# Kernel tuning notes

Measured on AMD Instinct MI355X. Metric: run time of the kernel, lower is better.

Reference implementation:

```python
import jax, jax.numpy as jnp
import numpy as np

N = 100000
E = 1600000
IN_C = 128
HID = 128
OUT_C = 2
EPS = 1e-5


def gcn_conv(x, src, dst, norm, W, b, num_nodes):
    # PyG GCNConv: linear transform then symmetric-normalized scatter-add
    h = x @ W                                  # [N, out]
    msg = h[src] * norm[:, None]               # [E+N, out] gather
    out = jax.ops.segment_sum(msg, dst, num_segments=num_nodes)
    return out + b


def batchnorm_eval(x, gamma, beta, rm, rv):
    inv = gamma / jnp.sqrt(rv + EPS)
    return (x - rm) * inv + beta


def setup_inputs() -> dict:
    key = jax.random.key(0)
    ks = jax.random.split(key, 16)
    x = jax.random.normal(ks[0], (N, IN_C), dtype=jnp.float32)
    edge_index = jax.random.randint(ks[1], (2, E), 0, N, dtype=jnp.int32)
    s = 1.0 / np.sqrt(IN_C)
    W1 = jax.random.uniform(ks[2], (IN_C, HID), jnp.float32, -s, s)
    b1 = jnp.zeros((HID,), jnp.float32)
    g1 = jnp.ones((HID,), jnp.float32)
    be1 = jnp.zeros((HID,), jnp.float32)
    rm1 = jax.random.normal(ks[3], (HID,), jnp.float32) * 0.1
    rv1 = jax.random.uniform(ks[4], (HID,), jnp.float32, 0.5, 1.5)
    s2 = 1.0 / np.sqrt(HID)
    W2 = jax.random.uniform(ks[5], (HID, HID), jnp.float32, -s2, s2)
    b2 = jnp.zeros((HID,), jnp.float32)
    g2 = jnp.ones((HID,), jnp.float32)
    be2 = jnp.zeros((HID,), jnp.float32)
    rm2 = jax.random.normal(ks[6], (HID,), jnp.float32) * 0.1
    rv2 = jax.random.uniform(ks[7], (HID,), jnp.float32, 0.5, 1.5)
    W3 = jax.random.uniform(ks[8], (HID, OUT_C), jnp.float32, -s2, s2)
    b3 = jnp.zeros((OUT_C,), jnp.float32)
    return {"x": x, "edge_index": edge_index,
            "W1": W1, "b1": b1, "g1": g1, "be1": be1, "rm1": rm1, "rv1": rv1,
            "W2": W2, "b2": b2, "g2": g2, "be2": be2, "rm2": rm2, "rv2": rv2,
            "W3": W3, "b3": b3}


def reference(x, edge_index, W1, b1, g1, be1, rm1, rv1,
              W2, b2, g2, be2, rm2, rv2, W3, b3):
    num_nodes = x.shape[0]
    loops = jnp.arange(num_nodes, dtype=edge_index.dtype)
    src = jnp.concatenate([edge_index[0], loops])   # add self loops
    dst = jnp.concatenate([edge_index[1], loops])
    deg = jax.ops.segment_sum(jnp.ones_like(dst, dtype=x.dtype), dst,
                              num_segments=num_nodes)
    dinv = jax.lax.rsqrt(deg)                        # deg >= 1 with self loops
    norm = dinv[src] * dinv[dst]                     # [E+N]

    h = gcn_conv(x, src, dst, norm, W1, b1, num_nodes)
    h = jax.nn.relu(batchnorm_eval(h, g1, be1, rm1, rv1))
    h = gcn_conv(h, src, dst, norm, W2, b2, num_nodes)
    h = jax.nn.relu(batchnorm_eval(h, g2, be2, rm2, rv2))
    out = gcn_conv(h, src, dst, norm, W3, b3, num_nodes)
    return out
```

## Files before the change

### kernel.cpp

```cpp
#include <hip/hip_runtime.h>

#define NN 100000
#define EE 1600000
#define CH 128

typedef _Float16 h2 __attribute__((ext_vector_type(2)));
typedef _Float16 h8 __attribute__((ext_vector_type(8)));
typedef float f32x4 __attribute__((ext_vector_type(4)));

#define S_NODES 512
#define NBUCK 196
#define CAP_E 10240


__global__ __launch_bounds__(256) void k_passA(const int* __restrict__ src, const int* __restrict__ dst,
                                               int* __restrict__ gcur, int* __restrict__ eb) {
    __shared__ int hist[NBUCK];
    __shared__ int curL[NBUCK];
    for (int t = threadIdx.x; t < NBUCK; t += 256) hist[t] = 0;
    __syncthreads();
    int base = blockIdx.x * 4096;
    int pk[16], bk[16];
#pragma unroll
    for (int j = 0; j < 16; ++j) {
        int i = base + threadIdx.x + 256 * j;
        if (i < EE) {
            int s = src[i], d = dst[i];
            bk[j] = d >> 9;
            pk[j] = (s << 9) | (d & 511);
            atomicAdd(&hist[bk[j]], 1);
        } else bk[j] = -1;
    }
    __syncthreads();
    for (int t = threadIdx.x; t < NBUCK; t += 256) {
        int h = hist[t];
        curL[t] = (h > 0) ? atomicAdd(&gcur[t], h) : 0;
    }
    __syncthreads();
#pragma unroll
    for (int j = 0; j < 16; ++j) {
        if (bk[j] >= 0) {
            int pos = atomicAdd(&curL[bk[j]], 1);
            if (pos < CAP_E) eb[bk[j] * CAP_E + pos] = pk[j];
        }
    }
}

__global__ __launch_bounds__(256) void k_passB1(const int* __restrict__ gcur, const int* __restrict__ eb,
                                                int* __restrict__ cnt) {
    __shared__ int c[S_NODES];
    int bId = blockIdx.x;
    for (int t = threadIdx.x; t < S_NODES; t += 256) c[t] = 0;
    __syncthreads();
    int n = min(gcur[bId], CAP_E);
    const int* e = eb + (size_t)bId * CAP_E;
    for (int i = threadIdx.x; i < n; i += 256) atomicAdd(&c[e[i] & 511], 1);
    __syncthreads();
    for (int t = threadIdx.x; t < S_NODES; t += 256) {
        int node = bId * S_NODES + t;
        if (node < NN) cnt[node] = c[t];
    }
}

__global__ __launch_bounds__(256) void k_passB2(const int* __restrict__ gcur, const int* __restrict__ eb,
                                                const int* __restrict__ rp, int* __restrict__ col) {
    __shared__ int start[S_NODES + 1];
    __shared__ int cur[S_NODES];
    __shared__ int stage[CAP_E + S_NODES];
    int bId = blockIdx.x;
    int nbase = bId * S_NODES;
    for (int t = threadIdx.x; t <= S_NODES; t += 256) {
        int node = nbase + t;
        start[t] = rp[node < NN ? node : NN];
    }
    __syncthreads();
    int base = start[0];
    for (int t = threadIdx.x; t < S_NODES; t += 256) cur[t] = start[t] - base;
    __syncthreads();
    int n = min(gcur[bId], CAP_E);
    const int* e = eb + (size_t)bId * CAP_E;
    for (int i = threadIdx.x; i < n; i += 256) {
        int pe = e[i];
        int pos = atomicAdd(&cur[pe & 511], 1);
        stage[pos] = pe >> 9;
    }
    for (int t = threadIdx.x; t < S_NODES; t += 256) {
        int node = nbase + t;
        if (node < NN) stage[start[t + 1] - 1 - base] = node;
    }
    __syncthreads();
    int total = start[S_NODES] - base;
    for (int i = threadIdx.x; i < total; i += 256) col[base + i] = stage[i];
}


__global__ __launch_bounds__(256) void k_scan1(const int* __restrict__ cnt, int* __restrict__ rp,
                                               int* __restrict__ bsum) {
    __shared__ int ts[256];
    int tid = threadIdx.x;
    int base = blockIdx.x * 1024 + tid * 4;
    int v[4]; int s = 0;
#pragma unroll
    for (int j = 0; j < 4; ++j) { int i = base + j; v[j] = s; s += (i < NN) ? (cnt[i] + 1) : 0; }
    ts[tid] = s; __syncthreads();
    for (int off = 1; off < 256; off <<= 1) {
        int t = (tid >= off) ? ts[tid - off] : 0;
        __syncthreads();
        ts[tid] += t;
        __syncthreads();
    }
    int excl = ts[tid] - s;
#pragma unroll
    for (int j = 0; j < 4; ++j) { int i = base + j; if (i < NN) rp[i] = excl + v[j]; }
    if (tid == 255) bsum[blockIdx.x] = ts[255];
}

__global__ __launch_bounds__(256) void k_scan2(int* __restrict__ bsum, int nb) {
    __shared__ int ts[256];
    int tid = threadIdx.x;
    int v = (tid < nb) ? bsum[tid] : 0;
    ts[tid] = v; __syncthreads();
    for (int off = 1; off < 256; off <<= 1) {
        int t = (tid >= off) ? ts[tid - off] : 0;
        __syncthreads();
        ts[tid] += t;
        __syncthreads();
    }
    if (tid < nb) bsum[tid] = ts[tid] - v;
}

__global__ __launch_bounds__(256) void k_scan3(int* __restrict__ rp, const int* __restrict__ bsum,
                                               const int* __restrict__ cnt, float* __restrict__ dinv) {
    int i = blockIdx.x * 256 + threadIdx.x;
    if (i < NN) {
        rp[i] += bsum[i >> 10];
        dinv[i] = rsqrtf((float)(cnt[i] + 1));
    }
    if (i == NN) rp[NN] = EE + NN;
}


__global__ __launch_bounds__(128) void k_bn(const float* __restrict__ b, const float* __restrict__ g,
                                            const float* __restrict__ be, const float* __restrict__ rm,
                                            const float* __restrict__ rv, float* __restrict__ sc,
                                            float* __restrict__ sh) {
    int t = threadIdx.x;
    float s = g[t] * rsqrtf(rv[t] + 1e-5f);
    sc[t] = s;
    sh[t] = (b[t] - rm[t]) * s + be[t];
}


__global__ __launch_bounds__(256) void k_cvt(const float* __restrict__ x, _Float16* __restrict__ xh) {
    int i = blockIdx.x * 256 + threadIdx.x;
    const float4* xv = (const float4*)x + (size_t)i * 2;
    float4 a = xv[0], b = xv[1];
    h8 o;
    o[0] = (_Float16)a.x; o[1] = (_Float16)a.y; o[2] = (_Float16)a.z; o[3] = (_Float16)a.w;
    o[4] = (_Float16)b.x; o[5] = (_Float16)b.y; o[6] = (_Float16)b.z; o[7] = (_Float16)b.w;
    *(h8*)(xh + (size_t)i * 8) = o;
}

__global__ __launch_bounds__(128) void k_prep_w(const float* __restrict__ W, _Float16* __restrict__ Wt) {
    int n = blockIdx.x, k = threadIdx.x;
    Wt[n * 128 + k] = (_Float16)W[k * 128 + n];
}


__global__ __launch_bounds__(256) void k_gemm_mfma(const _Float16* __restrict__ A,
                                                   const _Float16* __restrict__ Wt,
                                                   const float* __restrict__ dinv,
                                                   _Float16* __restrict__ C) {
    __shared__ _Float16 Wl[CH * CH];
    {
        const float4* wg = (const float4*)Wt;
#pragma unroll
        for (int i = 0; i < 8; ++i) {
            int chunk = i * 256 + threadIdx.x;
            int row = chunk >> 4, slot = chunk & 15;
            float4 v = wg[chunk];
            *(float4*)((char*)Wl + row * 256 + ((slot ^ (row & 15)) * 16)) = v;
        }
    }
    __syncthreads();
    int lane = threadIdx.x & 63;
    int l15 = lane & 15, lhi = lane >> 4;
    int row0 = blockIdx.x * 64 + (threadIdx.x >> 6) * 16;
    if (row0 >= NN) return;

    h8 afrag[4];
    const _Float16* Arow = A + (size_t)(row0 + l15) * CH + lhi * 8;
#pragma unroll
    for (int ks = 0; ks < 4; ++ks) afrag[ks] = *(const h8*)(Arow + ks * 32);

    f32x4 acc[8] = {};
#pragma unroll
    for (int ks = 0; ks < 4; ++ks) {
        int slot = ks * 4 + lhi;
#pragma unroll
        for (int c = 0; c < 8; ++c) {
            int brow = c * 16 + l15;
            h8 b = *(const h8*)((char*)Wl + brow * 256 + ((slot ^ (brow & 15)) * 16));
            acc[c] = __builtin_amdgcn_mfma_f32_16x16x32_f16(afrag[ks], b, acc[c], 0, 0, 0);
        }
    }
    float dv[4];
#pragma unroll
    for (int j = 0; j < 4; ++j) dv[j] = dinv[row0 + lhi * 4 + j];
#pragma unroll
    for (int c = 0; c < 8; ++c)
#pragma unroll
        for (int j = 0; j < 4; ++j) {
            float v = acc[c][j] * dv[j];
            C[(size_t)(row0 + lhi * 4 + j) * CH + c * 16 + l15] = (_Float16)v;
        }
}


__global__ __launch_bounds__(256) void k_agg128h(const _Float16* __restrict__ h, const int* __restrict__ rp,
                                                 const int* __restrict__ col, const float* __restrict__ dinv,
                                                 const float* __restrict__ sc, const float* __restrict__ sh,
                                                 _Float16* __restrict__ out) {
    int node = blockIdx.x * 4 + (threadIdx.x >> 6);
    if (node >= NN) return;
    node = __builtin_amdgcn_readfirstlane(node);
    int lane = threadIdx.x & 63;
    int beg = rp[node], end = rp[node + 1];
    float ax = 0.f, ay = 0.f;
    int e = beg;
    for (; e + 4 <= end; e += 4) {
        int s0 = col[e], s1 = col[e + 1], s2 = col[e + 2], s3 = col[e + 3];
        h2 v0 = *(const h2*)(h + (size_t)s0 * CH + lane * 2);
        h2 v1 = *(const h2*)(h + (size_t)s1 * CH + lane * 2);
        h2 v2 = *(const h2*)(h + (size_t)s2 * CH + lane * 2);
        h2 v3 = *(const h2*)(h + (size_t)s3 * CH + lane * 2);
        ax += (float)v0[0] + (float)v1[0] + (float)v2[0] + (float)v3[0];
        ay += (float)v0[1] + (float)v1[1] + (float)v2[1] + (float)v3[1];
    }
    for (; e < end; ++e) {
        int s0 = col[e];
        h2 v0 = *(const h2*)(h + (size_t)s0 * CH + lane * 2);
        ax += (float)v0[0];
        ay += (float)v0[1];
    }
    float dvn = dinv[node];
    int c = lane * 2;
    float2 scv = *(const float2*)(sc + c);
    float2 shv = *(const float2*)(sh + c);
    float o0 = fmaxf(fmaf(ax * dvn, scv.x, shv.x), 0.f);
    float o1 = fmaxf(fmaf(ay * dvn, scv.y, shv.y), 0.f);
    h2 o; o[0] = (_Float16)o0; o[1] = (_Float16)o1;
    *(h2*)(out + (size_t)node * CH + c) = o;
}


__global__ __launch_bounds__(256) void k_gemm_out(const _Float16* __restrict__ A, const float* __restrict__ W3,
                                                  const float* __restrict__ dinv, float* __restrict__ H3) {
    __shared__ float w3s[256];
    w3s[threadIdx.x] = W3[threadIdx.x];
    __syncthreads();
    int n = blockIdx.x * 256 + threadIdx.x;
    if (n >= NN) return;
    const h8* ar = (const h8*)(A + (size_t)n * CH);
    float a0 = 0.f, a1 = 0.f;
#pragma unroll
    for (int kb = 0; kb < 16; ++kb) {
        h8 a = ar[kb];
#pragma unroll
        for (int j = 0; j < 8; ++j) {
            float av = (float)a[j];
            int k = kb * 8 + j;
            a0 += av * w3s[k * 2];
            a1 += av * w3s[k * 2 + 1];
        }
    }
    float dv = dinv[n];
    *(float2*)(H3 + (size_t)n * 2) = make_float2(a0 * dv, a1 * dv);
}

__global__ __launch_bounds__(256) void k_agg_out(const float* __restrict__ H3, const int* __restrict__ rp,
                                                 const int* __restrict__ col, const float* __restrict__ dinv,
                                                 const float* __restrict__ b3, float* __restrict__ out) {
    int n = blockIdx.x * 256 + threadIdx.x;
    if (n >= NN) return;
    int beg = rp[n], end = rp[n + 1];
    float a0 = 0.f, a1 = 0.f;
    for (int e = beg; e < end; ++e) {
        int s = col[e];
        float2 hv = *(const float2*)(H3 + (size_t)s * 2);
        a0 += hv.x;
        a1 += hv.y;
    }
    float dv = dinv[n];
    out[(size_t)n * 2 + 0] = fmaf(a0, dv, b3[0]);
    out[(size_t)n * 2 + 1] = fmaf(a1, dv, b3[1]);
}


extern "C" void kernel_launch(void* const* d_in, const int* in_sizes, int n_in,
                              void* d_out, int out_size, void* d_ws, size_t ws_size,
                              hipStream_t stream) {
    const float* x  = (const float*)d_in[0];
    const int* ei   = (const int*)d_in[1];
    const int* src  = ei;
    const int* dst  = ei + EE;
    const float* W1 = (const float*)d_in[2];
    const float* b1 = (const float*)d_in[3];
    const float* g1 = (const float*)d_in[4];
    const float* be1 = (const float*)d_in[5];
    const float* rm1 = (const float*)d_in[6];
    const float* rv1 = (const float*)d_in[7];
    const float* W2 = (const float*)d_in[8];
    const float* b2 = (const float*)d_in[9];
    const float* g2 = (const float*)d_in[10];
    const float* be2 = (const float*)d_in[11];
    const float* rm2 = (const float*)d_in[12];
    const float* rv2 = (const float*)d_in[13];
    const float* W3 = (const float*)d_in[14];
    const float* b3 = (const float*)d_in[15];
    float* out = (float*)d_out;

    char* p = (char*)d_ws;
    auto carve = [&](size_t bytes) -> void* {
        void* r = (void*)p;
        p += (bytes + 255) & ~(size_t)255;
        return r;
    };
    int* cnt    = (int*)carve((size_t)NN * 4);
    int* rp     = (int*)carve((size_t)(NN + 1) * 4);
    float* dinv = (float*)carve((size_t)NN * 4);
    int* col    = (int*)carve((size_t)(EE + NN) * 4);
    int* bsum   = (int*)carve(1024 * 4);
    float* sc1  = (float*)carve(128 * 4);
    float* sh1  = (float*)carve(128 * 4);
    float* sc2  = (float*)carve(128 * 4);
    float* sh2  = (float*)carve(128 * 4);
    _Float16* bufA = (_Float16*)carve((size_t)NN * CH * 2);
    _Float16* bufB = (_Float16*)carve((size_t)NN * CH * 2);
    _Float16* xh   = (_Float16*)carve((size_t)NN * CH * 2);
    _Float16* Wt1  = (_Float16*)carve(128 * 128 * 2);
    _Float16* Wt2  = (_Float16*)carve(128 * 128 * 2);
    float* h3   = (float*)carve((size_t)NN * 2 * 4);

    int* eb   = (int*)bufA;
    int* gcur = eb + (size_t)NBUCK * CAP_E;

    hipMemsetAsync(gcur, 0, (size_t)NBUCK * 4, stream);

    int nb = (NN + 1023) / 1024;
    k_passA<<<(EE + 4095) / 4096, 256, 0, stream>>>(src, dst, gcur, eb);
    k_passB1<<<NBUCK, 256, 0, stream>>>(gcur, eb, cnt);
    k_scan1<<<nb, 256, 0, stream>>>(cnt, rp, bsum);
    k_scan2<<<1, 256, 0, stream>>>(bsum, nb);
    k_scan3<<<(NN + 256) / 256, 256, 0, stream>>>(rp, bsum, cnt, dinv);
    k_passB2<<<NBUCK, 256, 0, stream>>>(gcur, eb, rp, col);

    k_cvt<<<NN * CH / 8 / 256, 256, 0, stream>>>(x, xh);
    k_prep_w<<<128, 128, 0, stream>>>(W1, Wt1);
    k_prep_w<<<128, 128, 0, stream>>>(W2, Wt2);
    k_bn<<<1, 128, 0, stream>>>(b1, g1, be1, rm1, rv1, sc1, sh1);
    k_bn<<<1, 128, 0, stream>>>(b2, g2, be2, rm2, rv2, sc2, sh2);

    k_gemm_mfma<<<(NN + 63) / 64, 256, 0, stream>>>(xh, Wt1, dinv, bufA);
    k_agg128h<<<(NN + 3) / 4, 256, 0, stream>>>(bufA, rp, col, dinv, sc1, sh1, bufB);
    k_gemm_mfma<<<(NN + 63) / 64, 256, 0, stream>>>(bufB, Wt2, dinv, bufA);
    k_agg128h<<<(NN + 3) / 4, 256, 0, stream>>>(bufA, rp, col, dinv, sc2, sh2, bufB);
    k_gemm_out<<<(NN + 255) / 256, 256, 0, stream>>>(bufB, W3, dinv, h3);
    k_agg_out<<<(NN + 255) / 256, 256, 0, stream>>>(h3, rp, col, dinv, b3, out);
}
```

Before: 250.9 us.

## Fuse CSR build scans into bucket pass, fold fp32 conversion into first GEMM

The separate count, three-level scan and col-fill kernels are replaced by one tiny bucket-level scan plus a single per-bucket kernel. That kernel counts, does a local scan, writes rp and dinv, and scatters col. The x-to-fp16 conversion kernel is dropped by having the first GEMM read fp32 rows and convert in registers, and the weight-transpose and BN-prep launches are merged into one kernel. The gather loop in the 128-channel aggregation is unrolled to 8 edges for more memory-level parallelism. Together these cut kernel launches and a full fp16 copy of x, at the cost of wider fp32 loads in the first GEMM.

```diff
diff --git a/kernel.cpp b/kernel.cpp
--- a/kernel.cpp
+++ b/kernel.cpp
@@ -46,128 +46,106 @@
     }
 }
 
-__global__ __launch_bounds__(256) void k_passB1(const int* __restrict__ gcur, const int* __restrict__ eb,
-                                                int* __restrict__ cnt) {
+
+__global__ __launch_bounds__(256) void k_bscan(const int* __restrict__ gcur, int* __restrict__ bbase,
+                                               int* __restrict__ rp) {
+    __shared__ int ts[256];
+    int t = threadIdx.x;
+    int nn = (t < NBUCK) ? min(S_NODES, NN - t * S_NODES) : 0;
+    int v = (t < NBUCK) ? (min(gcur[t], CAP_E) + nn) : 0;
+    ts[t] = v; __syncthreads();
+    for (int off = 1; off < 256; off <<= 1) {
+        int u = (t >= off) ? ts[t - off] : 0;
+        __syncthreads();
+        ts[t] += u;
+        __syncthreads();
+    }
+    if (t < NBUCK) bbase[t] = ts[t] - v;
+    if (t == 0) rp[NN] = EE + NN;
+}
+
+
+__global__ __launch_bounds__(256) void k_passB(const int* __restrict__ gcur, const int* __restrict__ eb,
+                                               const int* __restrict__ bbase, int* __restrict__ rp,
+                                               float* __restrict__ dinv, int* __restrict__ col) {
     __shared__ int c[S_NODES];
-    int bId = blockIdx.x;
-    for (int t = threadIdx.x; t < S_NODES; t += 256) c[t] = 0;
-    __syncthreads();
-    int n = min(gcur[bId], CAP_E);
-    const int* e = eb + (size_t)bId * CAP_E;
-    for (int i = threadIdx.x; i < n; i += 256) atomicAdd(&c[e[i] & 511], 1);
-    __syncthreads();
-    for (int t = threadIdx.x; t < S_NODES; t += 256) {
-        int node = bId * S_NODES + t;
-        if (node < NN) cnt[node] = c[t];
-    }
-}
-
-__global__ __launch_bounds__(256) void k_passB2(const int* __restrict__ gcur, const int* __restrict__ eb,
-                                                const int* __restrict__ rp, int* __restrict__ col) {
-    __shared__ int start[S_NODES + 1];
+    __shared__ int excl[S_NODES];
     __shared__ int cur[S_NODES];
+    __shared__ int ts[256];
     __shared__ int stage[CAP_E + S_NODES];
     int bId = blockIdx.x;
     int nbase = bId * S_NODES;
-    for (int t = threadIdx.x; t <= S_NODES; t += 256) {
-        int node = nbase + t;
-        start[t] = rp[node < NN ? node : NN];
-    }
-    __syncthreads();
-    int base = start[0];
-    for (int t = threadIdx.x; t < S_NODES; t += 256) cur[t] = start[t] - base;
+    int tid = threadIdx.x;
+    c[tid] = 0; c[tid + 256] = 0;
     __syncthreads();
     int n = min(gcur[bId], CAP_E);
     const int* e = eb + (size_t)bId * CAP_E;
-    for (int i = threadIdx.x; i < n; i += 256) {
+    for (int i = tid; i < n; i += 256) atomicAdd(&c[e[i] & 511], 1);
+    __syncthreads();
+    int n0 = nbase + 2 * tid, n1 = n0 + 1;
+    int v0 = (n0 < NN) ? c[2 * tid] + 1 : 0;
+    int v1 = (n1 < NN) ? c[2 * tid + 1] + 1 : 0;
+    int s = v0 + v1;
+    ts[tid] = s; __syncthreads();
+    for (int off = 1; off < 256; off <<= 1) {
+        int u = (tid >= off) ? ts[tid - off] : 0;
+        __syncthreads();
+        ts[tid] += u;
+        __syncthreads();
+    }
+    int ex = ts[tid] - s;
+    int base = bbase[bId];
+    excl[2 * tid] = ex; excl[2 * tid + 1] = ex + v0;
+    cur[2 * tid] = ex;  cur[2 * tid + 1] = ex + v0;
+    if (n0 < NN) { rp[n0] = base + ex;      dinv[n0] = rsqrtf((float)v0); }
+    if (n1 < NN) { rp[n1] = base + ex + v0; dinv[n1] = rsqrtf((float)v1); }
+    __syncthreads();
+    for (int i = tid; i < n; i += 256) {
         int pe = e[i];
         int pos = atomicAdd(&cur[pe & 511], 1);
         stage[pos] = pe >> 9;
     }
-    for (int t = threadIdx.x; t < S_NODES; t += 256) {
-        int node = nbase + t;
-        if (node < NN) stage[start[t + 1] - 1 - base] = node;
-    }
-    __syncthreads();
-    int total = start[S_NODES] - base;
-    for (int i = threadIdx.x; i < total; i += 256) col[base + i] = stage[i];
-}
-
-
-__global__ __launch_bounds__(256) void k_scan1(const int* __restrict__ cnt, int* __restrict__ rp,
-                                               int* __restrict__ bsum) {
-    __shared__ int ts[256];
-    int tid = threadIdx.x;
-    int base = blockIdx.x * 1024 + tid * 4;
-    int v[4]; int s = 0;
-#pragma unroll
-    for (int j = 0; j < 4; ++j) { int i = base + j; v[j] = s; s += (i < NN) ? (cnt[i] + 1) : 0; }
-    ts[tid] = s; __syncthreads();
-    for (int off = 1; off < 256; off <<= 1) {
-        int t = (tid >= off) ? ts[tid - off] : 0;
-        __syncthreads();
-        ts[tid] += t;
-        __syncthreads();
-    }
-    int excl = ts[tid] - s;
-#pragma unroll
-    for (int j = 0; j < 4; ++j) { int i = base + j; if (i < NN) rp[i] = excl + v[j]; }
-    if (tid == 255) bsum[blockIdx.x] = ts[255];
-}
-
-__global__ __launch_bounds__(256) void k_scan2(int* __restrict__ bsum, int nb) {
-    __shared__ int ts[256];
-    int tid = threadIdx.x;
-    int v = (tid < nb) ? bsum[tid] : 0;
-    ts[tid] = v; __syncthreads();
-    for (int off = 1; off < 256; off <<= 1) {
-        int t = (tid >= off) ? ts[tid - off] : 0;
-        __syncthreads();
-        ts[tid] += t;
-        __syncthreads();
-    }
-    if (tid < nb) bsum[tid] = ts[tid] - v;
-}
-
-__global__ __launch_bounds__(256) void k_scan3(int* __restrict__ rp, const int* __restrict__ bsum,
-                                               const int* __restrict__ cnt, float* __restrict__ dinv) {
-    int i = blockIdx.x * 256 + threadIdx.x;
-    if (i < NN) {
-        rp[i] += bsum[i >> 10];
-        dinv[i] = rsqrtf((float)(cnt[i] + 1));
-    }
-    if (i == NN) rp[NN] = EE + NN;
-}
-
-
-__global__ __launch_bounds__(128) void k_bn(const float* __restrict__ b, const float* __restrict__ g,
-                                            const float* __restrict__ be, const float* __restrict__ rm,
-                                            const float* __restrict__ rv, float* __restrict__ sc,
-                                            float* __restrict__ sh) {
-    int t = threadIdx.x;
-    float s = g[t] * rsqrtf(rv[t] + 1e-5f);
-    sc[t] = s;
-    sh[t] = (b[t] - rm[t]) * s + be[t];
-}
-
-
-__global__ __launch_bounds__(256) void k_cvt(const float* __restrict__ x, _Float16* __restrict__ xh) {
-    int i = blockIdx.x * 256 + threadIdx.x;
-    const float4* xv = (const float4*)x + (size_t)i * 2;
-    float4 a = xv[0], b = xv[1];
-    h8 o;
-    o[0] = (_Float16)a.x; o[1] = (_Float16)a.y; o[2] = (_Float16)a.z; o[3] = (_Float16)a.w;
-    o[4] = (_Float16)b.x; o[5] = (_Float16)b.y; o[6] = (_Float16)b.z; o[7] = (_Float16)b.w;
-    *(h8*)(xh + (size_t)i * 8) = o;
-}
-
-__global__ __launch_bounds__(128) void k_prep_w(const float* __restrict__ W, _Float16* __restrict__ Wt) {
-    int n = blockIdx.x, k = threadIdx.x;
-    Wt[n * 128 + k] = (_Float16)W[k * 128 + n];
-}
-
-
-__global__ __launch_bounds__(256) void k_gemm_mfma(const _Float16* __restrict__ A,
+    {
+        int t0 = 2 * tid, t1 = 2 * tid + 1;
+        if (n0 < NN) stage[excl[t0] + c[t0]] = n0;
+        if (n1 < NN) stage[excl[t1] + c[t1]] = n1;
+    }
+    __syncthreads();
+    int total = ts[255];
+    for (int i = tid; i < total; i += 256) col[base + i] = stage[i];
+}
+
+
+__global__ __launch_bounds__(128) void k_prep(const float* __restrict__ W1, const float* __restrict__ W2,
+                                              _Float16* __restrict__ Wt1, _Float16* __restrict__ Wt2,
+                                              const float* __restrict__ b1, const float* __restrict__ g1,
+                                              const float* __restrict__ be1, const float* __restrict__ rm1,
+                                              const float* __restrict__ rv1,
+                                              const float* __restrict__ b2, const float* __restrict__ g2,
+                                              const float* __restrict__ be2, const float* __restrict__ rm2,
+                                              const float* __restrict__ rv2,
+                                              float* __restrict__ sc1, float* __restrict__ sh1,
+                                              float* __restrict__ sc2, float* __restrict__ sh2) {
+    int bid = blockIdx.x, t = threadIdx.x;
+    if (bid < 128) {
+        Wt1[bid * 128 + t] = (_Float16)W1[t * 128 + bid];
+    } else if (bid < 256) {
+        int nn = bid - 128;
+        Wt2[nn * 128 + t] = (_Float16)W2[t * 128 + nn];
+    } else if (bid == 256) {
+        float sv = g1[t] * rsqrtf(rv1[t] + 1e-5f);
+        sc1[t] = sv;
+        sh1[t] = (b1[t] - rm1[t]) * sv + be1[t];
+    } else {
+        float sv = g2[t] * rsqrtf(rv2[t] + 1e-5f);
+        sc2[t] = sv;
+        sh2[t] = (b2[t] - rm2[t]) * sv + be2[t];
+    }
+}
+
+
+template <bool F32IN>
+__global__ __launch_bounds__(256) void k_gemm_mfma(const void* __restrict__ Ain,
                                                    const _Float16* __restrict__ Wt,
                                                    const float* __restrict__ dinv,
                                                    _Float16* __restrict__ C) {
@@ -189,9 +167,22 @@
     if (row0 >= NN) return;
 
     h8 afrag[4];
-    const _Float16* Arow = A + (size_t)(row0 + l15) * CH + lhi * 8;
-#pragma unroll
-    for (int ks = 0; ks < 4; ++ks) afrag[ks] = *(const h8*)(Arow + ks * 32);
+    if (F32IN) {
+        const float* Arow = (const float*)Ain + (size_t)(row0 + l15) * CH + lhi * 8;
+#pragma unroll
+        for (int ks = 0; ks < 4; ++ks) {
+            float4 a = *(const float4*)(Arow + ks * 32);
+            float4 b = *(const float4*)(Arow + ks * 32 + 4);
+            h8 o;
+            o[0] = (_Float16)a.x; o[1] = (_Float16)a.y; o[2] = (_Float16)a.z; o[3] = (_Float16)a.w;
+            o[4] = (_Float16)b.x; o[5] = (_Float16)b.y; o[6] = (_Float16)b.z; o[7] = (_Float16)b.w;
+            afrag[ks] = o;
+        }
+    } else {
+        const _Float16* Arow = (const _Float16*)Ain + (size_t)(row0 + l15) * CH + lhi * 8;
+#pragma unroll
+        for (int ks = 0; ks < 4; ++ks) afrag[ks] = *(const h8*)(Arow + ks * 32);
+    }
 
     f32x4 acc[8] = {};
 #pragma unroll
@@ -228,14 +219,31 @@
     int beg = rp[node], end = rp[node + 1];
     float ax = 0.f, ay = 0.f;
     int e = beg;
-    for (; e + 4 <= end; e += 4) {
+    for (; e + 8 <= end; e += 8) {
+        int s0 = col[e], s1 = col[e + 1], s2 = col[e + 2], s3 = col[e + 3];
+        int s4 = col[e + 4], s5 = col[e + 5], s6 = col[e + 6], s7 = col[e + 7];
+        h2 v0 = *(const h2*)(h + (size_t)s0 * CH + lane * 2);
+        h2 v1 = *(const h2*)(h + (size_t)s1 * CH + lane * 2);
+        h2 v2 = *(const h2*)(h + (size_t)s2 * CH + lane * 2);
+        h2 v3 = *(const h2*)(h + (size_t)s3 * CH + lane * 2);
+        h2 v4 = *(const h2*)(h + (size_t)s4 * CH + lane * 2);
+        h2 v5 = *(const h2*)(h + (size_t)s5 * CH + lane * 2);
+        h2 v6 = *(const h2*)(h + (size_t)s6 * CH + lane * 2);
+        h2 v7 = *(const h2*)(h + (size_t)s7 * CH + lane * 2);
+        ax += ((float)v0[0] + (float)v1[0]) + ((float)v2[0] + (float)v3[0])
+            + ((float)v4[0] + (float)v5[0]) + ((float)v6[0] + (float)v7[0]);
+        ay += ((float)v0[1] + (float)v1[1]) + ((float)v2[1] + (float)v3[1])
+            + ((float)v4[1] + (float)v5[1]) + ((float)v6[1] + (float)v7[1]);
+    }
+    if (e + 4 <= end) {
         int s0 = col[e], s1 = col[e + 1], s2 = col[e + 2], s3 = col[e + 3];
         h2 v0 = *(const h2*)(h + (size_t)s0 * CH + lane * 2);
         h2 v1 = *(const h2*)(h + (size_t)s1 * CH + lane * 2);
         h2 v2 = *(const h2*)(h + (size_t)s2 * CH + lane * 2);
         h2 v3 = *(const h2*)(h + (size_t)s3 * CH + lane * 2);
-        ax += (float)v0[0] + (float)v1[0] + (float)v2[0] + (float)v3[0];
-        ay += (float)v0[1] + (float)v1[1] + (float)v2[1] + (float)v3[1];
+        ax += ((float)v0[0] + (float)v1[0]) + ((float)v2[0] + (float)v3[0]);
+        ay += ((float)v0[1] + (float)v1[1]) + ((float)v2[1] + (float)v3[1]);
+        e += 4;
     }
     for (; e < end; ++e) {
         int s0 = col[e];
@@ -326,18 +334,16 @@
         p += (bytes + 255) & ~(size_t)255;
         return r;
     };
-    int* cnt    = (int*)carve((size_t)NN * 4);
     int* rp     = (int*)carve((size_t)(NN + 1) * 4);
     float* dinv = (float*)carve((size_t)NN * 4);
     int* col    = (int*)carve((size_t)(EE + NN) * 4);
-    int* bsum   = (int*)carve(1024 * 4);
+    int* bbase  = (int*)carve(256 * 4);
     float* sc1  = (float*)carve(128 * 4);
     float* sh1  = (float*)carve(128 * 4);
     float* sc2  = (float*)carve(128 * 4);
     float* sh2  = (float*)carve(128 * 4);
     _Float16* bufA = (_Float16*)carve((size_t)NN * CH * 2);
     _Float16* bufB = (_Float16*)carve((size_t)NN * CH * 2);
-    _Float16* xh   = (_Float16*)carve((size_t)NN * CH * 2);
     _Float16* Wt1  = (_Float16*)carve(128 * 128 * 2);
     _Float16* Wt2  = (_Float16*)carve(128 * 128 * 2);
     float* h3   = (float*)carve((size_t)NN * 2 * 4);
@@ -347,23 +353,17 @@
 
     hipMemsetAsync(gcur, 0, (size_t)NBUCK * 4, stream);
 
-    int nb = (NN + 1023) / 1024;
     k_passA<<<(EE + 4095) / 4096, 256, 0, stream>>>(src, dst, gcur, eb);
-    k_passB1<<<NBUCK, 256, 0, stream>>>(gcur, eb, cnt);
-    k_scan1<<<nb, 256, 0, stream>>>(cnt, rp, bsum);
-    k_scan2<<<1, 256, 0, stream>>>(bsum, nb);
-    k_scan3<<<(NN + 256) / 256, 256, 0, stream>>>(rp, bsum, cnt, dinv);
-    k_passB2<<<NBUCK, 256, 0, stream>>>(gcur, eb, rp, col);
-
-    k_cvt<<<NN * CH / 8 / 256, 256, 0, stream>>>(x, xh);
-    k_prep_w<<<128, 128, 0, stream>>>(W1, Wt1);
-    k_prep_w<<<128, 128, 0, stream>>>(W2, Wt2);
-    k_bn<<<1, 128, 0, stream>>>(b1, g1, be1, rm1, rv1, sc1, sh1);
-    k_bn<<<1, 128, 0, stream>>>(b2, g2, be2, rm2, rv2, sc2, sh2);
-
-    k_gemm_mfma<<<(NN + 63) / 64, 256, 0, stream>>>(xh, Wt1, dinv, bufA);
+    k_bscan<<<1, 256, 0, stream>>>(gcur, bbase, rp);
+    k_passB<<<NBUCK, 256, 0, stream>>>(gcur, eb, bbase, rp, dinv, col);
+    k_prep<<<258, 128, 0, stream>>>(W1, W2, Wt1, Wt2,
+                                    b1, g1, be1, rm1, rv1,
+                                    b2, g2, be2, rm2, rv2,
+                                    sc1, sh1, sc2, sh2);
+
+    k_gemm_mfma<true><<<(NN + 63) / 64, 256, 0, stream>>>(x, Wt1, dinv, bufA);
     k_agg128h<<<(NN + 3) / 4, 256, 0, stream>>>(bufA, rp, col, dinv, sc1, sh1, bufB);
-    k_gemm_mfma<<<(NN + 63) / 64, 256, 0, stream>>>(bufB, Wt2, dinv, bufA);
+    k_gemm_mfma<false><<<(NN + 63) / 64, 256, 0, stream>>>(bufB, Wt2, dinv, bufA);
     k_agg128h<<<(NN + 3) / 4, 256, 0, stream>>>(bufA, rp, col, dinv, sc2, sh2, bufB);
     k_gemm_out<<<(NN + 255) / 256, 256, 0, stream>>>(bufB, W3, dinv, h3);
     k_agg_out<<<(NN + 255) / 256, 256, 0, stream>>>(h3, rp, col, dinv, b3, out);
```

Measured after the change: 228.0 us. 9.1% less time.
